# Kernel optimization log

Hardware: AMD Instinct MI355X
Metric: run time of the kernel (lower is better)

## Reference

```python
import jax, jax.numpy as jnp
import numpy as np

B, T, C_IN, C_HID, C_EMB, K, MAX_DUR = 16, 512, 512, 256, 384, 5, 8
MAX_MEL = T * MAX_DUR  # static upper bound on regulated length (4096)
LRELU_SLOPE = 0.3
PAD = (K - 1) // 2
EPS = 1e-5


def setup_inputs() -> dict:
    key = jax.random.key(0)
    ks = jax.random.split(key, 14)
    s = 0.05
    return {
        "x": jax.random.normal(ks[0], (B, T, C_IN), jnp.float32),
        "x_res": jax.random.normal(ks[1], (B, T, C_IN), jnp.float32),
        "duration_target": jax.random.randint(ks[2], (B, T), 0, MAX_DUR, dtype=jnp.int32),
        "embeddings": jax.random.normal(ks[3], (B, T, C_EMB), jnp.float32),
        "src_mask": jnp.zeros((B, T), jnp.bool_),
        "conv1_w": s * jax.random.normal(ks[4], (K, C_IN, C_HID), jnp.float32),
        "conv1_b": jnp.zeros((C_HID,), jnp.float32),
        "ln1_g": jnp.ones((C_HID,), jnp.float32),
        "ln1_b": jnp.zeros((C_HID,), jnp.float32),
        "conv2_w": s * jax.random.normal(ks[5], (K, C_HID, C_HID), jnp.float32),
        "conv2_b": jnp.zeros((C_HID,), jnp.float32),
        "ln2_g": jnp.ones((C_HID,), jnp.float32),
        "ln2_b": jnp.zeros((C_HID,), jnp.float32),
        "lin_w": s * jax.random.normal(ks[6], (C_HID, 1), jnp.float32),
        "lin_b": jnp.zeros((1,), jnp.float32),
    }


def _conv1d(x, w, b):
    # x: [B, T, Cin], w: [K, Cin, Cout] -> [B, T, Cout] (same padding)
    y = jax.lax.conv_general_dilated(
        x, w, window_strides=(1,), padding=[(PAD, PAD)],
        dimension_numbers=("NWC", "WIO", "NWC"))
    return y + b


def _layer_norm(x, g, b):
    mu = jnp.mean(x, axis=-1, keepdims=True)
    var = jnp.mean(jnp.square(x - mu), axis=-1, keepdims=True)
    return (x - mu) * jax.lax.rsqrt(var + EPS) * g + b


def _duration_predictor(x, mask, c1w, c1b, g1, b1, c2w, c2b, g2, b2, lw, lb):
    h = jax.nn.leaky_relu(_conv1d(x, c1w, c1b), LRELU_SLOPE)
    h = _layer_norm(h, g1, b1)  # dropout is identity at eval
    h = jax.nn.leaky_relu(_conv1d(h, c2w, c2b), LRELU_SLOPE)
    h = _layer_norm(h, g2, b2)
    h = (h @ lw + lb).squeeze(-1)  # [B, T]
    return jnp.where(mask, 0.0, h)


def _length_regulate(x, duration):
    # Fused prefix-sum + gather replacement for the looped expand/cat/pad.
    # token i occupies output frames [cumsum[i-1], cumsum[i])
    cum = jnp.cumsum(duration, axis=1)              # [B, T]
    total = cum[:, -1]                              # [B] mel lengths
    pos = jnp.arange(MAX_MEL, dtype=cum.dtype)      # [MAX_MEL]
    idx = jax.vmap(lambda c: jnp.searchsorted(c, pos, side="right"))(cum)  # [B, MAX_MEL]
    idx = jnp.clip(idx, 0, duration.shape[1] - 1)
    valid = (pos[None, :] < total[:, None])         # [B, MAX_MEL]
    out = jnp.take_along_axis(x, idx[..., None], axis=1)
    out = out * valid[..., None].astype(x.dtype)    # zero-padded past mel_len
    return out, total.astype(jnp.int32)


def reference(x, x_res, duration_target, embeddings, src_mask,
              conv1_w, conv1_b, ln1_g, ln1_b, conv2_w, conv2_b, ln2_g, ln2_b,
              lin_w, lin_b):
    # upsample_train path: x_res is detached before the duration predictor
    x_res = jax.lax.stop_gradient(x_res)
    log_duration_prediction = _duration_predictor(
        x_res, src_mask, conv1_w, conv1_b, ln1_g, ln1_b,
        conv2_w, conv2_b, ln2_g, ln2_b, lin_w, lin_b)
    x_up, _ = _length_regulate(x, duration_target)
    emb_up, _ = _length_regulate(embeddings, duration_target)
    return x_up, log_duration_prediction, emb_up
```

## Files before the change

### kernel.cpp

```cpp
#include <hip/hip_runtime.h>


constexpr int Bn = 16, Tn = 512, CIN1 = 512, CHID = 256, CEMB = 384, MAXMEL = 4096;
constexpr int NROWS = Bn * Tn;
#define LRELU 0.3f
#define EPSV 1e-5f

typedef __attribute__((ext_vector_type(8))) short bf16x8;
typedef __attribute__((ext_vector_type(4))) float f32x4;
typedef __attribute__((ext_vector_type(16))) float f32x16;
typedef __attribute__((ext_vector_type(4))) unsigned int u32x4;
typedef unsigned short ushort_t;

static __device__ __forceinline__ ushort_t f2bf(float f) {
  unsigned u = __builtin_bit_cast(unsigned, f);
  unsigned r = (u + 0x7fffu + ((u >> 16) & 1u)) >> 16;
  return (ushort_t)r;
}

template <int CI, bool F32IN>
static __device__ __forceinline__ void conv_body(
    int mt, int ns,
    const float* __restrict__ xin, const ushort_t* __restrict__ inbf,
    const ushort_t* __restrict__ wB, float* __restrict__ hraw) {
  constexpr int NCHUNK = CI / 128;
  constexpr int ROWS = 36, LDSTRIDE = 136;
  __shared__ ushort_t sA[ROWS * LDSTRIDE];

  const int b = mt >> 4, t0 = (mt & 15) * 32;
  const int tid = threadIdx.x;
  const int l = tid & 63, nh = tid >> 6;
  const int lm = l & 31, lq = l >> 5;
  const int cob32 = ns * 4 + nh;

  f32x16 acc;
#pragma unroll
  for (int i = 0; i < 16; ++i) acc[i] = 0.f;

  const ushort_t* pB = wB + (size_t)cob32 * 512 + l * 8;

  const int rbase = tid >> 6;
  const int c2 = (tid & 63) * 2;

#pragma unroll 1
  for (int chunk = 0; chunk < NCHUNK; ++chunk) {
    {
      const int cibase = chunk * 128;
      float2 rf[9];
      unsigned ru[9];
#pragma unroll
      for (int i = 0; i < 9; ++i) {
        const int r = i * 4 + rbase;
        const int t = t0 - 2 + r;
        if (F32IN) {
          rf[i] = make_float2(0.f, 0.f);
          if ((unsigned)t < (unsigned)Tn)
            rf[i] = *(const float2*)(xin + (size_t)(b * Tn + t) * CI + cibase + c2);
        } else {
          ru[i] = 0u;
          if ((unsigned)t < (unsigned)Tn)
            ru[i] = *(const unsigned*)(inbf + (size_t)(b * Tn + t) * CI + cibase + c2);
        }
      }
#pragma unroll
      for (int i = 0; i < 9; ++i) {
        const int r = i * 4 + rbase;
        unsigned hv;
        if (F32IN)
          hv = (unsigned)f2bf(rf[i].x) | ((unsigned)f2bf(rf[i].y) << 16);
        else
          hv = ru[i];
        const int sw = ((r >> 3) & 3) << 3;
        *(unsigned*)&sA[r * LDSTRIDE + (c2 ^ sw)] = hv;
      }
    }
    __syncthreads();

#pragma unroll 1
    for (int ksh = 0; ksh < 5; ++ksh) {
      const int r = lm + ksh;
      const int sw = ((r >> 3) & 3) << 3;
      const size_t bbase = (size_t)((ksh * (CI / 16) + chunk * 8) * 8) * 512;
#pragma unroll
      for (int kk = 0; kk < 8; ++kk) {
        const int c = (kk * 16 + lq * 8) ^ sw;
        const bf16x8 a = *(const bf16x8*)&sA[r * LDSTRIDE + c];
        const bf16x8 bv = *(const bf16x8*)(pB + bbase + (size_t)kk * 8 * 512);
        acc = __builtin_amdgcn_mfma_f32_32x32x16_bf16(a, bv, acc, 0, 0, 0);
      }
    }
    __syncthreads();
  }

  const int col = ns * 128 + nh * 32 + lm;
  float* pOut = hraw + (size_t)(b * Tn + t0) * 256 + col;
#pragma unroll
  for (int reg = 0; reg < 16; ++reg) {
    const int row = (reg & 3) + 8 * (reg >> 2) + 4 * lq;
    pOut[(size_t)row * 256] = acc[reg];
  }
}

__global__ __launch_bounds__(256, 2) void conv1_gather_kernel(
    const float* __restrict__ x_res, const ushort_t* __restrict__ w1,
    float* __restrict__ hraw,
    const float* __restrict__ x, const int* __restrict__ idx,
    float* __restrict__ x_up) {
  const int blk = blockIdx.x;
  if (blk % 3 == 0) {
    const int cid = blk / 3;
    conv_body<512, true>(cid & 255, cid >> 8, x_res, nullptr, w1, hraw);
    return;
  }
  const int gid = blk - 1 - blk / 3;
  const f32x4* x4 = (const f32x4*)x;
  f32x4* xu4 = (f32x4*)x_up;
  const int tid0 = gid * 256 + threadIdx.x;
  constexpr int stride = 1024 * 256;
  const f32x4 z = (f32x4){0.f, 0.f, 0.f, 0.f};
#pragma unroll 1
  for (int k0 = 0; k0 < 32; k0 += 4) {
    int tv[4];
#pragma unroll
    for (int j = 0; j < 4; ++j)
      tv[j] = idx[(tid0 + (k0 + j) * stride) >> 7];
    f32x4 v[4];
#pragma unroll
    for (int j = 0; j < 4; ++j) {
      const int u = tid0 + (k0 + j) * stride;
      const int i = u & 127;
      const int b = u >> 19;
      v[j] = (tv[j] >= 0) ? x4[((b << 9) + tv[j]) * 128 + i] : z;
    }
#pragma unroll
    for (int j = 0; j < 4; ++j)
      __builtin_nontemporal_store(v[j], &xu4[tid0 + (k0 + j) * stride]);
  }
}

__global__ __launch_bounds__(256, 2) void conv2_gather_kernel(
    const ushort_t* __restrict__ h1, const ushort_t* __restrict__ w2,
    float* __restrict__ hraw,
    const float* __restrict__ emb, const int* __restrict__ idx,
    float* __restrict__ emb_up) {
  const int blk = blockIdx.x;
  if (blk % 3 == 0) {
    const int cid = blk / 3;
    conv_body<256, false>(cid & 255, cid >> 8, nullptr, h1, w2, hraw);
    return;
  }
  const int gid = blk - 1 - blk / 3;
  const f32x4* e4 = (const f32x4*)emb;
  f32x4* eu4 = (f32x4*)emb_up;
  const int tid0 = gid * 256 + threadIdx.x;
  constexpr int stride = 1024 * 256;
  const f32x4 z = (f32x4){0.f, 0.f, 0.f, 0.f};
#pragma unroll 1
  for (int k0 = 0; k0 < 24; k0 += 4) {
    int tv[4];
    int bp[4];
#pragma unroll
    for (int j = 0; j < 4; ++j) {
      const int u = tid0 + (k0 + j) * stride;
      bp[j] = u / 96;
      tv[j] = idx[bp[j]];
    }
    f32x4 v[4];
#pragma unroll
    for (int j = 0; j < 4; ++j) {
      const int u = tid0 + (k0 + j) * stride;
      const int i = u - bp[j] * 96;
      const int b = bp[j] >> 12;
      v[j] = (tv[j] >= 0) ? e4[((b << 9) + tv[j]) * 96 + i] : z;
    }
#pragma unroll
    for (int j = 0; j < 4; ++j)
      __builtin_nontemporal_store(v[j], &eu4[tid0 + (k0 + j) * stride]);
  }
}

template <bool FINAL>
__global__ __launch_bounds__(256) void ln_kernel(
    const float* __restrict__ hraw,
    const float* __restrict__ bias, const float* __restrict__ g,
    const float* __restrict__ be, ushort_t* __restrict__ h1,
    const float* __restrict__ lw, const float* __restrict__ lb,
    const unsigned char* __restrict__ mask, float* __restrict__ ldp) {
  const int row = blockIdx.x * 4 + (threadIdx.x >> 6);
  const int l = threadIdx.x & 63;
  const f32x4 p = ((const f32x4*)hraw)[row * 64 + l];
  const f32x4 bi = ((const f32x4*)bias)[l];
  float v0 = p.x + bi.x, v1 = p.y + bi.y, v2 = p.z + bi.z, v3 = p.w + bi.w;
  v0 = (v0 > 0.f) ? v0 : LRELU * v0;
  v1 = (v1 > 0.f) ? v1 : LRELU * v1;
  v2 = (v2 > 0.f) ? v2 : LRELU * v2;
  v3 = (v3 > 0.f) ? v3 : LRELU * v3;
  float s = v0 + v1 + v2 + v3;
  float s2 = v0 * v0 + v1 * v1 + v2 * v2 + v3 * v3;
#pragma unroll
  for (int off = 32; off >= 1; off >>= 1) {
    s += __shfl_xor(s, off);
    s2 += __shfl_xor(s2, off);
  }
  const float mu = s * (1.f / 256.f);
  const float var = s2 * (1.f / 256.f) - mu * mu;
  const float rs = rsqrtf(var + EPSV);
  const f32x4 gg = ((const f32x4*)g)[l];
  const f32x4 bb = ((const f32x4*)be)[l];
  const float h0 = (v0 - mu) * rs * gg.x + bb.x;
  const float h1v = (v1 - mu) * rs * gg.y + bb.y;
  const float h2 = (v2 - mu) * rs * gg.z + bb.z;
  const float h3 = (v3 - mu) * rs * gg.w + bb.w;
  if (!FINAL) {
    ushort4 uh;
    uh.x = f2bf(h0); uh.y = f2bf(h1v); uh.z = f2bf(h2); uh.w = f2bf(h3);
    ((ushort4*)h1)[row * 64 + l] = uh;
  } else {
    const f32x4 lv = ((const f32x4*)lw)[l];
    float d = h0 * lv.x + h1v * lv.y + h2 * lv.z + h3 * lv.w;
#pragma unroll
    for (int off = 32; off >= 1; off >>= 1) d += __shfl_xor(d, off);
    if (l == 0) {
      float val = d + lb[0];
      if (mask[row]) val = 0.f;
      ldp[row] = val;
    }
  }
}

__global__ __launch_bounds__(512) void prep_kernel(
    const float* __restrict__ w1src, const float* __restrict__ w2src,
    ushort_t* __restrict__ w1dst, ushort_t* __restrict__ w2dst,
    const int* __restrict__ dur, int* __restrict__ idx) {
  __shared__ int wsum[8];
  const int blk = blockIdx.x;
  const int tid = threadIdx.x;
  if (blk < 240) {
    const float* src;
    ushort_t* dst;
    int CI, fr, sh;
    const int wv = tid >> 6, l = tid & 63;
    if (blk < 160) { src = w1src; dst = w1dst; CI = 512; sh = 5; fr = blk * 8 + wv; }
    else           { src = w2src; dst = w2dst; CI = 256; sh = 4; fr = (blk - 160) * 8 + wv; }
    const int cob32 = fr & 7;
    const int t = fr >> 3;
    const int ksh = t >> sh;
    const int ci16 = t & ((1 << sh) - 1);
    const int ci = ci16 * 16 + (l >> 5) * 8;
    const int co = cob32 * 32 + (l & 31);
    ushort_t v[8];
#pragma unroll
    for (int j = 0; j < 8; ++j)
      v[j] = f2bf(src[((size_t)(ksh * CI + ci + j)) * 256 + co]);
    u32x4 pack;
#pragma unroll
    for (int q = 0; q < 4; ++q)
      pack[q] = (unsigned)v[q * 2] | ((unsigned)v[q * 2 + 1] << 16);
    *(u32x4*)&dst[(size_t)fr * 512 + l * 8] = pack;
    return;
  }
  const int b = blk - 240;
  const int lane = tid & 63, wv = tid >> 6;
  const int d = dur[b * Tn + tid];
  int v = d;
#pragma unroll
  for (int off = 1; off <= 32; off <<= 1) {
    const int t = __shfl_up(v, off);
    if (lane >= off) v += t;
  }
  if (lane == 63) wsum[wv] = v;
  __syncthreads();
  int woff = 0, total = 0;
#pragma unroll
  for (int i = 0; i < 8; ++i) {
    const int s = wsum[i];
    if (i < wv) woff += s;
    total += s;
  }
  const int end = v + woff;
  for (int p = end - d; p < end; ++p) idx[b * MAXMEL + p] = tid;
  for (int p = total + tid; p < MAXMEL; p += 512) idx[b * MAXMEL + p] = -1;
}

extern "C" void kernel_launch(void* const* d_in, const int* in_sizes, int n_in,
                              void* d_out, int out_size, void* d_ws, size_t ws_size,
                              hipStream_t stream) {
  const float* x     = (const float*)d_in[0];
  const float* x_res = (const float*)d_in[1];
  const int*   dur   = (const int*)d_in[2];
  const float* emb   = (const float*)d_in[3];
  const unsigned char* mask = (const unsigned char*)d_in[4];
  const float* c1w = (const float*)d_in[5];
  const float* c1b = (const float*)d_in[6];
  const float* g1  = (const float*)d_in[7];
  const float* b1  = (const float*)d_in[8];
  const float* c2w = (const float*)d_in[9];
  const float* c2b = (const float*)d_in[10];
  const float* g2  = (const float*)d_in[11];
  const float* b2  = (const float*)d_in[12];
  const float* lw  = (const float*)d_in[13];
  const float* lb  = (const float*)d_in[14];

  float* x_up   = (float*)d_out;
  float* ldp    = x_up + (size_t)Bn * MAXMEL * CIN1;
  float* emb_up = ldp + (size_t)Bn * Tn;

  int* idx = (int*)d_ws;
  ushort_t* h1 = (ushort_t*)((char*)d_ws + (size_t)Bn * MAXMEL * 4);
  ushort_t* w1 = h1 + (size_t)NROWS * 256;
  ushort_t* w2 = w1 + (size_t)5 * 512 * 256;
  float* hraw = (float*)(w2 + (size_t)5 * 256 * 256);

  prep_kernel<<<256, 512, 0, stream>>>(c1w, c2w, w1, w2, dur, idx);
  conv1_gather_kernel<<<1536, 256, 0, stream>>>(
      x_res, w1, hraw, x, idx, x_up);
  ln_kernel<false><<<NROWS / 4, 256, 0, stream>>>(
      hraw, c1b, g1, b1, h1, nullptr, nullptr, nullptr, nullptr);
  conv2_gather_kernel<<<1536, 256, 0, stream>>>(
      h1, w2, hraw, emb, idx, emb_up);
  ln_kernel<true><<<NROWS / 4, 256, 0, stream>>>(
      hraw, c2b, g2, b2, nullptr, lw, lb, mask, ldp);
}
```

Baseline: 343.1 us.

## Fuse conv, layernorm and gather stages into one cooperative persistent kernel

```diff
diff --git a/kernel.cpp b/kernel.cpp
--- a/kernel.cpp
+++ b/kernel.cpp
@@ -1,4 +1,7 @@
 #include <hip/hip_runtime.h>
+#include <hip/hip_cooperative_groups.h>
+
+namespace cg = cooperative_groups;
 
 
 constexpr int Bn = 16, Tn = 512, CIN1 = 512, CHID = 256, CEMB = 384, MAXMEL = 4096;
@@ -101,131 +104,159 @@
   }
 }
 
-__global__ __launch_bounds__(256, 2) void conv1_gather_kernel(
-    const float* __restrict__ x_res, const ushort_t* __restrict__ w1,
-    float* __restrict__ hraw,
-    const float* __restrict__ x, const int* __restrict__ idx,
+static __device__ __forceinline__ void xup_slice(
+    int cid, const float* __restrict__ x, const int* __restrict__ idx,
     float* __restrict__ x_up) {
-  const int blk = blockIdx.x;
-  if (blk % 3 == 0) {
-    const int cid = blk / 3;
-    conv_body<512, true>(cid & 255, cid >> 8, x_res, nullptr, w1, hraw);
-    return;
-  }
-  const int gid = blk - 1 - blk / 3;
   const f32x4* x4 = (const f32x4*)x;
   f32x4* xu4 = (f32x4*)x_up;
-  const int tid0 = gid * 256 + threadIdx.x;
-  constexpr int stride = 1024 * 256;
+  const int base = cid * 16384 + threadIdx.x;
   const f32x4 z = (f32x4){0.f, 0.f, 0.f, 0.f};
 #pragma unroll 1
-  for (int k0 = 0; k0 < 32; k0 += 4) {
+  for (int k0 = 0; k0 < 64; k0 += 4) {
     int tv[4];
 #pragma unroll
     for (int j = 0; j < 4; ++j)
-      tv[j] = idx[(tid0 + (k0 + j) * stride) >> 7];
+      tv[j] = idx[(base + (k0 + j) * 256) >> 7];
     f32x4 v[4];
 #pragma unroll
     for (int j = 0; j < 4; ++j) {
-      const int u = tid0 + (k0 + j) * stride;
+      const int u = base + (k0 + j) * 256;
       const int i = u & 127;
       const int b = u >> 19;
       v[j] = (tv[j] >= 0) ? x4[((b << 9) + tv[j]) * 128 + i] : z;
     }
 #pragma unroll
     for (int j = 0; j < 4; ++j)
-      __builtin_nontemporal_store(v[j], &xu4[tid0 + (k0 + j) * stride]);
-  }
-}
-
-__global__ __launch_bounds__(256, 2) void conv2_gather_kernel(
-    const ushort_t* __restrict__ h1, const ushort_t* __restrict__ w2,
-    float* __restrict__ hraw,
-    const float* __restrict__ emb, const int* __restrict__ idx,
-    float* __restrict__ emb_up) {
-  const int blk = blockIdx.x;
-  if (blk % 3 == 0) {
-    const int cid = blk / 3;
-    conv_body<256, false>(cid & 255, cid >> 8, nullptr, h1, w2, hraw);
-    return;
-  }
-  const int gid = blk - 1 - blk / 3;
+      __builtin_nontemporal_store(v[j], &xu4[base + (k0 + j) * 256]);
+  }
+}
+
+static __device__ __forceinline__ void emb_slice(
+    int cid, int klo, int khi, const float* __restrict__ emb,
+    const int* __restrict__ idx, float* __restrict__ emb_up) {
   const f32x4* e4 = (const f32x4*)emb;
   f32x4* eu4 = (f32x4*)emb_up;
-  const int tid0 = gid * 256 + threadIdx.x;
-  constexpr int stride = 1024 * 256;
+  const int base = cid * 12288 + threadIdx.x;
   const f32x4 z = (f32x4){0.f, 0.f, 0.f, 0.f};
 #pragma unroll 1
-  for (int k0 = 0; k0 < 24; k0 += 4) {
-    int tv[4];
-    int bp[4];
+  for (int k0 = klo; k0 < khi; k0 += 4) {
+    int tv[4], bp[4];
 #pragma unroll
     for (int j = 0; j < 4; ++j) {
-      const int u = tid0 + (k0 + j) * stride;
+      const int u = base + (k0 + j) * 256;
       bp[j] = u / 96;
       tv[j] = idx[bp[j]];
     }
     f32x4 v[4];
 #pragma unroll
     for (int j = 0; j < 4; ++j) {
-      const int u = tid0 + (k0 + j) * stride;
+      const int u = base + (k0 + j) * 256;
       const int i = u - bp[j] * 96;
       const int b = bp[j] >> 12;
       v[j] = (tv[j] >= 0) ? e4[((b << 9) + tv[j]) * 96 + i] : z;
     }
 #pragma unroll
     for (int j = 0; j < 4; ++j)
-      __builtin_nontemporal_store(v[j], &eu4[tid0 + (k0 + j) * stride]);
+      __builtin_nontemporal_store(v[j], &eu4[base + (k0 + j) * 256]);
   }
 }
 
 template <bool FINAL>
-__global__ __launch_bounds__(256) void ln_kernel(
-    const float* __restrict__ hraw,
+static __device__ __forceinline__ void ln_rows(
+    int cid, const float* __restrict__ hraw,
     const float* __restrict__ bias, const float* __restrict__ g,
     const float* __restrict__ be, ushort_t* __restrict__ h1,
     const float* __restrict__ lw, const float* __restrict__ lb,
     const unsigned char* __restrict__ mask, float* __restrict__ ldp) {
-  const int row = blockIdx.x * 4 + (threadIdx.x >> 6);
   const int l = threadIdx.x & 63;
-  const f32x4 p = ((const f32x4*)hraw)[row * 64 + l];
-  const f32x4 bi = ((const f32x4*)bias)[l];
-  float v0 = p.x + bi.x, v1 = p.y + bi.y, v2 = p.z + bi.z, v3 = p.w + bi.w;
-  v0 = (v0 > 0.f) ? v0 : LRELU * v0;
-  v1 = (v1 > 0.f) ? v1 : LRELU * v1;
-  v2 = (v2 > 0.f) ? v2 : LRELU * v2;
-  v3 = (v3 > 0.f) ? v3 : LRELU * v3;
-  float s = v0 + v1 + v2 + v3;
-  float s2 = v0 * v0 + v1 * v1 + v2 * v2 + v3 * v3;
-#pragma unroll
-  for (int off = 32; off >= 1; off >>= 1) {
-    s += __shfl_xor(s, off);
-    s2 += __shfl_xor(s2, off);
-  }
-  const float mu = s * (1.f / 256.f);
-  const float var = s2 * (1.f / 256.f) - mu * mu;
-  const float rs = rsqrtf(var + EPSV);
-  const f32x4 gg = ((const f32x4*)g)[l];
-  const f32x4 bb = ((const f32x4*)be)[l];
-  const float h0 = (v0 - mu) * rs * gg.x + bb.x;
-  const float h1v = (v1 - mu) * rs * gg.y + bb.y;
-  const float h2 = (v2 - mu) * rs * gg.z + bb.z;
-  const float h3 = (v3 - mu) * rs * gg.w + bb.w;
-  if (!FINAL) {
-    ushort4 uh;
-    uh.x = f2bf(h0); uh.y = f2bf(h1v); uh.z = f2bf(h2); uh.w = f2bf(h3);
-    ((ushort4*)h1)[row * 64 + l] = uh;
+#pragma unroll 1
+  for (int pass = 0; pass < 4; ++pass) {
+    const int row = cid * 16 + pass * 4 + (threadIdx.x >> 6);
+    const f32x4 p = ((const f32x4*)hraw)[row * 64 + l];
+    const f32x4 bi = ((const f32x4*)bias)[l];
+    float v0 = p.x + bi.x, v1 = p.y + bi.y, v2 = p.z + bi.z, v3 = p.w + bi.w;
+    v0 = (v0 > 0.f) ? v0 : LRELU * v0;
+    v1 = (v1 > 0.f) ? v1 : LRELU * v1;
+    v2 = (v2 > 0.f) ? v2 : LRELU * v2;
+    v3 = (v3 > 0.f) ? v3 : LRELU * v3;
+    float s = v0 + v1 + v2 + v3;
+    float s2 = v0 * v0 + v1 * v1 + v2 * v2 + v3 * v3;
+#pragma unroll
+    for (int off = 32; off >= 1; off >>= 1) {
+      s += __shfl_xor(s, off);
+      s2 += __shfl_xor(s2, off);
+    }
+    const float mu = s * (1.f / 256.f);
+    const float var = s2 * (1.f / 256.f) - mu * mu;
+    const float rs = rsqrtf(var + EPSV);
+    const f32x4 gg = ((const f32x4*)g)[l];
+    const f32x4 bb = ((const f32x4*)be)[l];
+    const float h0 = (v0 - mu) * rs * gg.x + bb.x;
+    const float h1v = (v1 - mu) * rs * gg.y + bb.y;
+    const float h2 = (v2 - mu) * rs * gg.z + bb.z;
+    const float h3 = (v3 - mu) * rs * gg.w + bb.w;
+    if (!FINAL) {
+      ushort4 uh;
+      uh.x = f2bf(h0); uh.y = f2bf(h1v); uh.z = f2bf(h2); uh.w = f2bf(h3);
+      ((ushort4*)h1)[row * 64 + l] = uh;
+    } else {
+      const f32x4 lv = ((const f32x4*)lw)[l];
+      float d = h0 * lv.x + h1v * lv.y + h2 * lv.z + h3 * lv.w;
+#pragma unroll
+      for (int off = 32; off >= 1; off >>= 1) d += __shfl_xor(d, off);
+      if (l == 0) {
+        float val = d + lb[0];
+        if (mask[row]) val = 0.f;
+        ldp[row] = val;
+      }
+    }
+  }
+}
+
+__global__ __launch_bounds__(256, 2) void mega_kernel(
+    const float* __restrict__ x_res, const ushort_t* __restrict__ w1,
+    float* __restrict__ hraw,
+    const float* __restrict__ x, const int* __restrict__ idx,
+    float* __restrict__ x_up,
+    const float* __restrict__ c1b, const float* __restrict__ g1,
+    const float* __restrict__ b1, ushort_t* __restrict__ h1,
+    const float* __restrict__ emb, float* __restrict__ emb_up,
+    const ushort_t* __restrict__ w2, const float* __restrict__ c2b,
+    const float* __restrict__ g2, const float* __restrict__ b2,
+    const float* __restrict__ lw, const float* __restrict__ lb,
+    const unsigned char* __restrict__ mask, float* __restrict__ ldp) {
+  cg::grid_group grid = cg::this_grid();
+  const int cid = blockIdx.x;
+  const bool gfirst = (((cid >> 8) ^ cid) & 1) != 0;
+
+  if (gfirst) {
+    xup_slice(cid, x, idx, x_up);
+    conv_body<512, true>(cid & 255, cid >> 8, x_res, nullptr, w1, hraw);
   } else {
-    const f32x4 lv = ((const f32x4*)lw)[l];
-    float d = h0 * lv.x + h1v * lv.y + h2 * lv.z + h3 * lv.w;
-#pragma unroll
-    for (int off = 32; off >= 1; off >>= 1) d += __shfl_xor(d, off);
-    if (l == 0) {
-      float val = d + lb[0];
-      if (mask[row]) val = 0.f;
-      ldp[row] = val;
-    }
-  }
+    conv_body<512, true>(cid & 255, cid >> 8, x_res, nullptr, w1, hraw);
+    xup_slice(cid, x, idx, x_up);
+  }
+  grid.sync();
+
+  if (gfirst) {
+    emb_slice(cid, 0, 32, emb, idx, emb_up);
+    ln_rows<false>(cid, hraw, c1b, g1, b1, h1, nullptr, nullptr, nullptr, nullptr);
+  } else {
+    ln_rows<false>(cid, hraw, c1b, g1, b1, h1, nullptr, nullptr, nullptr, nullptr);
+    emb_slice(cid, 0, 32, emb, idx, emb_up);
+  }
+  grid.sync();
+
+  if (gfirst) {
+    emb_slice(cid, 32, 48, emb, idx, emb_up);
+    conv_body<256, false>(cid & 255, cid >> 8, nullptr, h1, w2, hraw);
+  } else {
+    conv_body<256, false>(cid & 255, cid >> 8, nullptr, h1, w2, hraw);
+    emb_slice(cid, 32, 48, emb, idx, emb_up);
+  }
+  grid.sync();
+
+  ln_rows<true>(cid, hraw, c2b, g2, b2, nullptr, lw, lb, mask, ldp);
 }
 
 __global__ __launch_bounds__(512) void prep_kernel(
@@ -312,12 +343,12 @@
   float* hraw = (float*)(w2 + (size_t)5 * 256 * 256);
 
   prep_kernel<<<256, 512, 0, stream>>>(c1w, c2w, w1, w2, dur, idx);
-  conv1_gather_kernel<<<1536, 256, 0, stream>>>(
-      x_res, w1, hraw, x, idx, x_up);
-  ln_kernel<false><<<NROWS / 4, 256, 0, stream>>>(
-      hraw, c1b, g1, b1, h1, nullptr, nullptr, nullptr, nullptr);
-  conv2_gather_kernel<<<1536, 256, 0, stream>>>(
-      h1, w2, hraw, emb, idx, emb_up);
-  ln_kernel<true><<<NROWS / 4, 256, 0, stream>>>(
-      hraw, c2b, g2, b2, nullptr, lw, lb, mask, ldp);
-}
+
+  void* args[] = {
+      (void*)&x_res, (void*)&w1, (void*)&hraw, (void*)&x, (void*)&idx,
+      (void*)&x_up, (void*)&c1b, (void*)&g1, (void*)&b1, (void*)&h1,
+      (void*)&emb, (void*)&emb_up, (void*)&w2, (void*)&c2b, (void*)&g2,
+      (void*)&b2, (void*)&lw, (void*)&lb, (void*)&mask, (void*)&ldp};
+  hipLaunchCooperativeKernel((const void*)mega_kernel, dim3(512), dim3(256),
+                             args, 0, stream);
+}
```

New measurement: 586.8 us. +71.0%, slower.

## Fuse bias, LeakyReLU and LayerNorm epilogues into conv kernels with full-width tiles

Applied to the files above, without the earlier changes.

```diff
diff --git a/kernel.cpp b/kernel.cpp
--- a/kernel.cpp
+++ b/kernel.cpp
@@ -18,26 +18,34 @@
   return (ushort_t)r;
 }
 
-template <int CI, bool F32IN>
-static __device__ __forceinline__ void conv_body(
-    int mt, int ns,
+template <int CI, bool F32IN, bool FINAL>
+static __device__ __forceinline__ void conv_fused_body(
+    int mt,
     const float* __restrict__ xin, const ushort_t* __restrict__ inbf,
-    const ushort_t* __restrict__ wB, float* __restrict__ hraw) {
+    const ushort_t* __restrict__ wB,
+    const float* __restrict__ bias, const float* __restrict__ g,
+    const float* __restrict__ be, ushort_t* __restrict__ h1out,
+    const float* __restrict__ lw, const float* __restrict__ lb,
+    const unsigned char* __restrict__ mask, float* __restrict__ ldp) {
   constexpr int NCHUNK = CI / 128;
   constexpr int ROWS = 36, LDSTRIDE = 136;
   __shared__ ushort_t sA[ROWS * LDSTRIDE];
+  __shared__ float sred[32][4];
+  __shared__ float s2red[32][4];
+  __shared__ float smu[32];
+  __shared__ float srs[32];
 
   const int b = mt >> 4, t0 = (mt & 15) * 32;
   const int tid = threadIdx.x;
   const int l = tid & 63, nh = tid >> 6;
   const int lm = l & 31, lq = l >> 5;
-  const int cob32 = ns * 4 + nh;
-
-  f32x16 acc;
-#pragma unroll
-  for (int i = 0; i < 16; ++i) acc[i] = 0.f;
-
-  const ushort_t* pB = wB + (size_t)cob32 * 512 + l * 8;
+
+  f32x16 acc0, acc1;
+#pragma unroll
+  for (int i = 0; i < 16; ++i) { acc0[i] = 0.f; acc1[i] = 0.f; }
+
+  const ushort_t* pB0 = wB + (size_t)nh * 512 + l * 8;
+  const ushort_t* pB1 = wB + (size_t)(nh + 4) * 512 + l * 8;
 
   const int rbase = tid >> 6;
   const int c2 = (tid & 63) * 2;
@@ -85,34 +93,117 @@
       for (int kk = 0; kk < 8; ++kk) {
         const int c = (kk * 16 + lq * 8) ^ sw;
         const bf16x8 a = *(const bf16x8*)&sA[r * LDSTRIDE + c];
-        const bf16x8 bv = *(const bf16x8*)(pB + bbase + (size_t)kk * 8 * 512);
-        acc = __builtin_amdgcn_mfma_f32_32x32x16_bf16(a, bv, acc, 0, 0, 0);
+        const bf16x8 bv0 = *(const bf16x8*)(pB0 + bbase + (size_t)kk * 8 * 512);
+        const bf16x8 bv1 = *(const bf16x8*)(pB1 + bbase + (size_t)kk * 8 * 512);
+        acc0 = __builtin_amdgcn_mfma_f32_32x32x16_bf16(a, bv0, acc0, 0, 0, 0);
+        acc1 = __builtin_amdgcn_mfma_f32_32x32x16_bf16(a, bv1, acc1, 0, 0, 0);
       }
     }
     __syncthreads();
   }
 
-  const int col = ns * 128 + nh * 32 + lm;
-  float* pOut = hraw + (size_t)(b * Tn + t0) * 256 + col;
-#pragma unroll
-  for (int reg = 0; reg < 16; ++reg) {
-    const int row = (reg & 3) + 8 * (reg >> 2) + 4 * lq;
-    pOut[(size_t)row * 256] = acc[reg];
+  const int col0 = nh * 32 + lm;
+  const int col1 = col0 + 128;
+  const float bi0 = bias[col0], bi1 = bias[col1];
+  float s[16], s2v[16];
+#pragma unroll
+  for (int rg = 0; rg < 16; ++rg) {
+    float a0 = acc0[rg] + bi0;
+    float a1 = acc1[rg] + bi1;
+    a0 = (a0 > 0.f) ? a0 : LRELU * a0;
+    a1 = (a1 > 0.f) ? a1 : LRELU * a1;
+    acc0[rg] = a0;
+    acc1[rg] = a1;
+    s[rg] = a0 + a1;
+    s2v[rg] = a0 * a0 + a1 * a1;
+  }
+#pragma unroll
+  for (int off = 16; off >= 1; off >>= 1) {
+#pragma unroll
+    for (int rg = 0; rg < 16; ++rg) {
+      s[rg] += __shfl_xor(s[rg], off);
+      s2v[rg] += __shfl_xor(s2v[rg], off);
+    }
+  }
+  if (lm == 0) {
+#pragma unroll
+    for (int rg = 0; rg < 16; ++rg) {
+      const int row = (rg & 3) + 8 * (rg >> 2) + 4 * lq;
+      sred[row][nh] = s[rg];
+      s2red[row][nh] = s2v[rg];
+    }
+  }
+  __syncthreads();
+  if (tid < 32) {
+    float a = 0.f, q = 0.f;
+#pragma unroll
+    for (int w = 0; w < 4; ++w) { a += sred[tid][w]; q += s2red[tid][w]; }
+    const float mu = a * (1.f / 256.f);
+    const float var = q * (1.f / 256.f) - mu * mu;
+    smu[tid] = mu;
+    srs[tid] = rsqrtf(var + EPSV);
+  }
+  __syncthreads();
+
+  const float g0 = g[col0], g1v = g[col1];
+  const float be0 = be[col0], be1 = be[col1];
+  if constexpr (!FINAL) {
+    ushort_t* po = h1out + (size_t)(b * Tn + t0) * 256;
+#pragma unroll
+    for (int rg = 0; rg < 16; ++rg) {
+      const int row = (rg & 3) + 8 * (rg >> 2) + 4 * lq;
+      const float mu = smu[row], rs = srs[row];
+      po[(size_t)row * 256 + col0] = f2bf((acc0[rg] - mu) * rs * g0 + be0);
+      po[(size_t)row * 256 + col1] = f2bf((acc1[rg] - mu) * rs * g1v + be1);
+    }
+  } else {
+    const float w0 = lw[col0], w1v = lw[col1];
+    float d[16];
+#pragma unroll
+    for (int rg = 0; rg < 16; ++rg) {
+      const int row = (rg & 3) + 8 * (rg >> 2) + 4 * lq;
+      const float mu = smu[row], rs = srs[row];
+      const float h0 = (acc0[rg] - mu) * rs * g0 + be0;
+      const float h1v = (acc1[rg] - mu) * rs * g1v + be1;
+      d[rg] = h0 * w0 + h1v * w1v;
+    }
+#pragma unroll
+    for (int off = 16; off >= 1; off >>= 1) {
+#pragma unroll
+      for (int rg = 0; rg < 16; ++rg) d[rg] += __shfl_xor(d[rg], off);
+    }
+    __syncthreads();
+    if (lm == 0) {
+#pragma unroll
+      for (int rg = 0; rg < 16; ++rg) {
+        const int row = (rg & 3) + 8 * (rg >> 2) + 4 * lq;
+        sred[row][nh] = d[rg];
+      }
+    }
+    __syncthreads();
+    if (tid < 32) {
+      float a = lb[0];
+#pragma unroll
+      for (int w = 0; w < 4; ++w) a += sred[tid][w];
+      const int grow = b * Tn + t0 + tid;
+      ldp[grow] = mask[grow] ? 0.f : a;
+    }
   }
 }
 
 __global__ __launch_bounds__(256, 2) void conv1_gather_kernel(
     const float* __restrict__ x_res, const ushort_t* __restrict__ w1,
-    float* __restrict__ hraw,
+    const float* __restrict__ c1b, const float* __restrict__ g1,
+    const float* __restrict__ b1, ushort_t* __restrict__ h1,
     const float* __restrict__ x, const int* __restrict__ idx,
     float* __restrict__ x_up) {
   const int blk = blockIdx.x;
-  if (blk % 3 == 0) {
-    const int cid = blk / 3;
-    conv_body<512, true>(cid & 255, cid >> 8, x_res, nullptr, w1, hraw);
+  if (blk % 5 == 0) {
+    conv_fused_body<512, true, false>(blk / 5, x_res, nullptr, w1, c1b, g1, b1,
+                                      h1, nullptr, nullptr, nullptr, nullptr);
     return;
   }
-  const int gid = blk - 1 - blk / 3;
+  const int gid = blk - 1 - blk / 5;
   const f32x4* x4 = (const f32x4*)x;
   f32x4* xu4 = (f32x4*)x_up;
   const int tid0 = gid * 256 + threadIdx.x;
@@ -140,16 +231,19 @@
 
 __global__ __launch_bounds__(256, 2) void conv2_gather_kernel(
     const ushort_t* __restrict__ h1, const ushort_t* __restrict__ w2,
-    float* __restrict__ hraw,
+    const float* __restrict__ c2b, const float* __restrict__ g2,
+    const float* __restrict__ b2, const float* __restrict__ lw,
+    const float* __restrict__ lb, const unsigned char* __restrict__ mask,
+    float* __restrict__ ldp,
     const float* __restrict__ emb, const int* __restrict__ idx,
     float* __restrict__ emb_up) {
   const int blk = blockIdx.x;
-  if (blk % 3 == 0) {
-    const int cid = blk / 3;
-    conv_body<256, false>(cid & 255, cid >> 8, nullptr, h1, w2, hraw);
+  if (blk % 5 == 0) {
+    conv_fused_body<256, false, true>(blk / 5, nullptr, h1, w2, c2b, g2, b2,
+                                      nullptr, lw, lb, mask, ldp);
     return;
   }
-  const int gid = blk - 1 - blk / 3;
+  const int gid = blk - 1 - blk / 5;
   const f32x4* e4 = (const f32x4*)emb;
   f32x4* eu4 = (f32x4*)emb_up;
   const int tid0 = gid * 256 + threadIdx.x;
@@ -176,55 +270,6 @@
 #pragma unroll
     for (int j = 0; j < 4; ++j)
       __builtin_nontemporal_store(v[j], &eu4[tid0 + (k0 + j) * stride]);
-  }
-}
-
-template <bool FINAL>
-__global__ __launch_bounds__(256) void ln_kernel(
-    const float* __restrict__ hraw,
-    const float* __restrict__ bias, const float* __restrict__ g,
-    const float* __restrict__ be, ushort_t* __restrict__ h1,
-    const float* __restrict__ lw, const float* __restrict__ lb,
-    const unsigned char* __restrict__ mask, float* __restrict__ ldp) {
-  const int row = blockIdx.x * 4 + (threadIdx.x >> 6);
-  const int l = threadIdx.x & 63;
-  const f32x4 p = ((const f32x4*)hraw)[row * 64 + l];
-  const f32x4 bi = ((const f32x4*)bias)[l];
-  float v0 = p.x + bi.x, v1 = p.y + bi.y, v2 = p.z + bi.z, v3 = p.w + bi.w;
-  v0 = (v0 > 0.f) ? v0 : LRELU * v0;
-  v1 = (v1 > 0.f) ? v1 : LRELU * v1;
-  v2 = (v2 > 0.f) ? v2 : LRELU * v2;
-  v3 = (v3 > 0.f) ? v3 : LRELU * v3;
-  float s = v0 + v1 + v2 + v3;
-  float s2 = v0 * v0 + v1 * v1 + v2 * v2 + v3 * v3;
-#pragma unroll
-  for (int off = 32; off >= 1; off >>= 1) {
-    s += __shfl_xor(s, off);
-    s2 += __shfl_xor(s2, off);
-  }
-  const float mu = s * (1.f / 256.f);
-  const float var = s2 * (1.f / 256.f) - mu * mu;
-  const float rs = rsqrtf(var + EPSV);
-  const f32x4 gg = ((const f32x4*)g)[l];
-  const f32x4 bb = ((const f32x4*)be)[l];
-  const float h0 = (v0 - mu) * rs * gg.x + bb.x;
-  const float h1v = (v1 - mu) * rs * gg.y + bb.y;
-  const float h2 = (v2 - mu) * rs * gg.z + bb.z;
-  const float h3 = (v3 - mu) * rs * gg.w + bb.w;
-  if (!FINAL) {
-    ushort4 uh;
-    uh.x = f2bf(h0); uh.y = f2bf(h1v); uh.z = f2bf(h2); uh.w = f2bf(h3);
-    ((ushort4*)h1)[row * 64 + l] = uh;
-  } else {
-    const f32x4 lv = ((const f32x4*)lw)[l];
-    float d = h0 * lv.x + h1v * lv.y + h2 * lv.z + h3 * lv.w;
-#pragma unroll
-    for (int off = 32; off >= 1; off >>= 1) d += __shfl_xor(d, off);
-    if (l == 0) {
-      float val = d + lb[0];
-      if (mask[row]) val = 0.f;
-      ldp[row] = val;
-    }
   }
 }
 
@@ -309,15 +354,10 @@
   ushort_t* h1 = (ushort_t*)((char*)d_ws + (size_t)Bn * MAXMEL * 4);
   ushort_t* w1 = h1 + (size_t)NROWS * 256;
   ushort_t* w2 = w1 + (size_t)5 * 512 * 256;
-  float* hraw = (float*)(w2 + (size_t)5 * 256 * 256);
 
   prep_kernel<<<256, 512, 0, stream>>>(c1w, c2w, w1, w2, dur, idx);
-  conv1_gather_kernel<<<1536, 256, 0, stream>>>(
-      x_res, w1, hraw, x, idx, x_up);
-  ln_kernel<false><<<NROWS / 4, 256, 0, stream>>>(
-      hraw, c1b, g1, b1, h1, nullptr, nullptr, nullptr, nullptr);
-  conv2_gather_kernel<<<1536, 256, 0, stream>>>(
-      h1, w2, hraw, emb, idx, emb_up);
-  ln_kernel<true><<<NROWS / 4, 256, 0, stream>>>(
-      hraw, c2b, g2, b2, nullptr, lw, lb, mask, ldp);
-}
+  conv1_gather_kernel<<<1280, 256, 0, stream>>>(
+      x_res, w1, c1b, g1, b1, h1, x, idx, x_up);
+  conv2_gather_kernel<<<1280, 256, 0, stream>>>(
+      h1, w2, c2b, g2, b2, lw, lb, mask, ldp, emb, idx, emb_up);
+}
```

Result: slower. 355.1 us (+3.5%).
